# Performance work log

Measured on AMD Instinct MI355X. Metric: run time of the kernel, lower is better.

## Reference

```python
import jax, jax.numpy as jnp
import numpy as np

BETA = 0.25


def setup_inputs() -> dict:
    key = jax.random.key(0)
    k1, k2 = jax.random.split(key)
    z = jax.random.normal(k1, (16, 256, 32, 32), dtype=jnp.float32)
    # nn.Embedding init: uniform(-1/K, 1/K) with K = in_channels = 16384
    K, D = 16384, 256
    emb = jax.random.uniform(k2, (K, D), dtype=jnp.float32,
                             minval=-1.0 / K, maxval=1.0 / K)
    return {"z": z, "emb": emb}


def reference(z, emb):
    K, D = emb.shape
    # NCHW -> NHWC, flatten to tokens
    zp = jnp.transpose(z, (0, 2, 3, 1))            # [B,H,W,D]
    zf = zp.reshape(-1, D)                          # [N,D]
    # squared L2 distances: ||z||^2 + ||e||^2 - 2 z.e  -> [N,K]
    d = (jnp.sum(zf * zf, axis=1, keepdims=True)
         + jnp.sum(emb * emb, axis=1)
         - 2.0 * jnp.matmul(zf, emb.T))
    idx = jnp.argmin(d, axis=1)                     # [N] int
    # gather via direct lookup (equivalent to one-hot @ emb)
    z_q = emb[idx].reshape(zp.shape)                # [B,H,W,D]
    # commitment + codebook loss
    loss = (jnp.mean((jax.lax.stop_gradient(z_q) - zp) ** 2)
            + BETA * jnp.mean((z_q - jax.lax.stop_gradient(zp)) ** 2))
    # perplexity from code usage histogram (same as mean of one-hot rows)
    counts = jax.ops.segment_sum(jnp.ones_like(idx, dtype=jnp.float32), idx,
                                 num_segments=K)
    e_mean = counts / idx.shape[0]
    perplexity = jnp.exp(-jnp.sum(e_mean * jnp.log(e_mean + 1e-10)))
    # straight-through estimator, back to NCHW
    z_q_st = zp + jax.lax.stop_gradient(z_q - zp)
    z_q_out = jnp.transpose(z_q_st, (0, 3, 1, 2))   # [B,D,H,W]
    return z_q_out, loss, perplexity, idx
```

## Files before the change

kernel.cpp:

```cpp
#include <hip/hip_runtime.h>
#include <math.h>

#define NTOK   16384
#define DDIM   256
#define HWD    1024
#define CHW    262144
#define MARGIN 3.0e-4f
#define CLIPF  5.5f
#define QS     (127.0f/5.5f)
#define EQS    2080768.0f
#define SCALE  (5.5f/(127.0f*127.0f*16384.0f))

#define WS_TI8   0u
#define WS_CI8   4194304u
#define WS_M1    8388608u
#define WS_M2    16777216u
#define WS_ARG   25165824u
#define WS_FLG   29360128u
#define WS_EE    29376512u
#define WS_ZZ    29442048u
#define WS_IDX   29507584u
#define WS_CNT   29573120u
#define WS_LSUM  29638656u

typedef __attribute__((ext_vector_type(4)))  int   i32x4;
typedef __attribute__((ext_vector_type(16))) char  c16;
typedef __attribute__((ext_vector_type(4)))  _Float16 h4;

__device__ __forceinline__ void top2m(int& a1, int& a2, const int b1, const int b2) {
  const int mn = min(a1, b1);
  a1 = max(a1, b1);
  a2 = max(max(a2, b2), mn);
}

__global__ __launch_bounds__(256) void k_prep(const float* __restrict__ z,
                                              const float* __restrict__ emb,
                                              char* __restrict__ Ti8,
                                              char* __restrict__ Ci8,
                                              float* __restrict__ zz,
                                              float* __restrict__ ee,
                                              float* __restrict__ zt,
                                              unsigned char* __restrict__ flags) {
  const int bid = blockIdx.x;
  const int tid = threadIdx.x;
  const int t64 = tid & 63, chunk = tid >> 6;
  if (bid < 256) {
    __shared__ double part[4][64];
    __shared__ int   fpart[4][64];
    const int n = bid * 64 + t64;
    const int b = n >> 10, hw = n & 1023;
    const float* zp = z + (size_t)b * CHW + hw;
    float tmp[64];
    double s = 0.0;
    int clip = 0;
    #pragma unroll
    for (int j = 0; j < 64; ++j) {
      const float f = zp[(size_t)(chunk * 64 + j) * HWD];
      tmp[j] = f;
      s += (double)f * (double)f;
      clip |= (fabsf(f) > CLIPF) ? 1 : 0;
    }
    c16 q[4];
    #pragma unroll
    for (int sl = 0; sl < 4; ++sl)
      #pragma unroll
      for (int j = 0; j < 16; ++j)
        q[sl][j] = (char)(int)rintf(fminf(fmaxf(tmp[sl * 16 + j], -CLIPF), CLIPF) * QS);
    const int rl = n & 127, tile = n >> 7;
    char* dst = Ti8 + (size_t)tile * 32768 + chunk * 8192 + rl * 64;
    const int sw = ((rl >> 1) & 3) << 4;
    #pragma unroll
    for (int sl = 0; sl < 4; ++sl) *(c16*)(dst + ((sl * 16) ^ sw)) = q[sl];
    float* ztp = zt + (size_t)n * 256 + chunk * 64;
    #pragma unroll
    for (int j4 = 0; j4 < 16; ++j4) *(float4*)(ztp + j4 * 4) = *(float4*)&tmp[j4 * 4];
    part[chunk][t64] = s;
    fpart[chunk][t64] = clip;
    __syncthreads();
    if (tid < 64) {
      zz[n] = (float)(part[0][t64] + part[1][t64] + part[2][t64] + part[3][t64]);
      flags[n] = (unsigned char)(fpart[0][t64] | fpart[1][t64] | fpart[2][t64] | fpart[3][t64]);
    }
  } else {
    __shared__ float rows[64][257];
    __shared__ double part2[4][64];
    const int k0 = (bid - 256) * 64;
    for (int i = tid; i < 16384; i += 256)
      rows[i >> 8][i & 255] = emb[(size_t)k0 * DDIM + i];
    __syncthreads();
    const int code = k0 + t64;
    double s = 0.0;
    c16 q[4];
    #pragma unroll
    for (int sl = 0; sl < 4; ++sl)
      #pragma unroll
      for (int j = 0; j < 16; ++j) {
        const float f = rows[t64][chunk * 64 + sl * 16 + j];
        q[sl][j] = (char)(int)rintf(f * EQS);
        s += (double)f * (double)f;
      }
    char* dst = Ci8 + (size_t)code * 256 + chunk * 64;
    #pragma unroll
    for (int sl = 0; sl < 4; ++sl) *(c16*)(dst + sl * 16) = q[sl];
    part2[chunk][t64] = s;
    __syncthreads();
    if (tid < 64)
      ee[code] = (float)(part2[0][t64] + part2[1][t64] + part2[2][t64] + part2[3][t64]);
  }
}

__global__ __launch_bounds__(256) void k_mdist(
    const char* __restrict__ tokimg, const char* __restrict__ codrows,
    _Float16* __restrict__ M1, _Float16* __restrict__ M2,
    unsigned char* __restrict__ ARG) {
  __shared__ __attribute__((aligned(16))) char ldsB[65536];
  __shared__ _Float16 m1l[2][256];
  __shared__ _Float16 m2l[2][256];
  __shared__ unsigned char agl[2][256];
  const int raw = blockIdx.x;
  const int p = raw & 7;
  const int ctile = p * 16 + ((raw >> 3) & 15);
  const int tgrp = raw >> 7;
  const int tid = threadIdx.x;
  const int w = tid >> 6, lane = tid & 63;
  const int wr = w >> 1, wc = w & 1;
  const int fr = lane & 15, fq = lane >> 4;

  i32x4 afr[4][4];
  {
    const char* ab = codrows + (size_t)(ctile * 128 + wr * 64 + fr) * 256 + fq * 16;
    #pragma unroll
    for (int m = 0; m < 4; ++m)
      #pragma unroll
      for (int kc = 0; kc < 4; ++kc)
        afr[m][kc] = *(const i32x4*)(ab + m * 16 * 256 + kc * 64);
  }

  int boff[4][4];
  #pragma unroll
  for (int n = 0; n < 4; ++n)
    #pragma unroll
    for (int kc = 0; kc < 4; ++kc) {
      const int t = wc * 64 + n * 16 + fr;
      boff[n][kc] = kc * 8192 + t * 64 + ((fq * 16) ^ (((t >> 1) & 3) << 4));
    }

  #define STAGEB(buf, tt)                                                             \
    {                                                                                 \
      const char* src = tokimg + (size_t)(tt) * 32768;                                \
      char* dstb = ldsB + (buf) * 32768;                                              \
      _Pragma("unroll")                                                               \
      for (int r = 0; r < 8; ++r) {                                                   \
        const int u = r * 256 + tid;                                                  \
        __builtin_amdgcn_global_load_lds(                                             \
            (const __attribute__((address_space(1))) void*)(src + u * 16),            \
            (__attribute__((address_space(3))) void*)(dstb + u * 16), 16, 0, 0);      \
      }                                                                               \
    }

  STAGEB(0, tgrp * 8);
  __syncthreads();

  const int fq4 = fq * 4;
  for (int it = 0; it < 8; ++it) {
    const int pb = it & 1;
    const int ttile = tgrp * 8 + it;
    if (it < 7) STAGEB(pb ^ 1, ttile + 1);
    const char* bufb = ldsB + pb * 32768;

    i32x4 acc[4][4];
    #pragma unroll
    for (int m = 0; m < 4; ++m)
      #pragma unroll
      for (int n = 0; n < 4; ++n) acc[m][n] = (i32x4)0;

    __builtin_amdgcn_s_setprio(1);
    #pragma unroll
    for (int kc = 0; kc < 4; ++kc) {
      i32x4 b[4];
      #pragma unroll
      for (int n = 0; n < 4; ++n) b[n] = *(const i32x4*)(bufb + boff[n][kc]);
      #pragma unroll
      for (int m = 0; m < 4; ++m)
        #pragma unroll
        for (int n = 0; n < 4; ++n)
          acc[m][n] = __builtin_amdgcn_mfma_i32_16x16x64_i8(afr[m][kc], b[n], acc[m][n], 0, 0, 0);
    }
    __builtin_amdgcn_s_setprio(0);

    #pragma unroll
    for (int n = 0; n < 4; ++n) {
      int p1[8], p2[8];
      #pragma unroll
      for (int m = 0; m < 4; ++m)
        #pragma unroll
        for (int jj = 0; jj < 2; ++jj) {
          const int k0 = (acc[m][n][2 * jj]     << 8) | (m * 16 + fq4 + 2 * jj);
          const int k1 = (acc[m][n][2 * jj + 1] << 8) | (m * 16 + fq4 + 2 * jj + 1);
          p1[m * 2 + jj] = max(k0, k1);
          p2[m * 2 + jj] = min(k0, k1);
        }
      top2m(p1[0], p2[0], p1[1], p2[1]); top2m(p1[2], p2[2], p1[3], p2[3]);
      top2m(p1[4], p2[4], p1[5], p2[5]); top2m(p1[6], p2[6], p1[7], p2[7]);
      top2m(p1[0], p2[0], p1[2], p2[2]); top2m(p1[4], p2[4], p1[6], p2[6]);
      top2m(p1[0], p2[0], p1[4], p2[4]);
      int k1 = p1[0], k2 = p2[0];
      #pragma unroll
      for (int off = 16; off <= 32; off <<= 1) {
        const int o1 = __shfl_xor(k1, off, 64);
        const int o2 = __shfl_xor(k2, off, 64);
        top2m(k1, k2, o1, o2);
      }
      if (lane < 16) {
        const int tl = wc * 64 + n * 16 + fr;
        m1l[pb][tl * 2 + wr] = (_Float16)(-2.0f * SCALE * (float)(k1 >> 8));
        m2l[pb][tl * 2 + wr] = (_Float16)(-2.0f * SCALE * (float)(k2 >> 8));
        agl[pb][tl * 2 + wr] = (unsigned char)(k1 & 255);
      }
    }
    __syncthreads();
    if (tid < 128) {
      const int tok = ttile * 128 + tid;
      *(unsigned int*)((char*)M1 + (size_t)tok * 512 + ctile * 4) =
          *(const unsigned int*)(&m1l[pb][tid * 2]);
      M2[(size_t)(ctile * 2) * NTOK + tok]     = m2l[pb][tid * 2];
      M2[(size_t)(ctile * 2 + 1) * NTOK + tok] = m2l[pb][tid * 2 + 1];
      ARG[(size_t)(ctile * 2) * NTOK + tok]     = agl[pb][tid * 2];
      ARG[(size_t)(ctile * 2 + 1) * NTOK + tok] = agl[pb][tid * 2 + 1];
    }
  }
}

__global__ __launch_bounds__(256) void k_pick(
    const float* __restrict__ zt, const float* __restrict__ emb,
    const float* __restrict__ zz, const float* __restrict__ ee,
    const _Float16* __restrict__ M1, const _Float16* __restrict__ M2,
    const unsigned char* __restrict__ ARG, const unsigned char* __restrict__ flags,
    int* __restrict__ idx, float* __restrict__ out_idxf,
    int* __restrict__ counts, double* __restrict__ lsum) {
  __shared__ float zrow[4][260];
  __shared__ int   clist[4][576];
  __shared__ int   wcnt[4];
  __shared__ double wsum[4];
  const int tid = threadIdx.x;
  const int w = tid >> 6, lane = tid & 63;
  const int g16 = lane >> 4, l16 = lane & 15;
  double dsum = 0.0;
  for (int ni = 0; ni < 2; ++ni) {
    const int n = blockIdx.x * 8 + w * 2 + ni;
    if (lane == 0) wcnt[w] = 0;
    *(float4*)&zrow[w][lane * 4] = *(const float4*)(zt + (size_t)n * 256 + lane * 4);
    const h4 mv = *(const h4*)(M1 + (size_t)n * 256 + lane * 4);
    float ta4[4];
    #pragma unroll
    for (int s = 0; s < 4; ++s) ta4[s] = (float)mv[s];
    float mr = fminf(fminf(ta4[0], ta4[1]), fminf(ta4[2], ta4[3]));
    #pragma unroll
    for (int o = 32; o; o >>= 1) mr = fminf(mr, __shfl_xor(mr, o, 64));
    const int ex0 = flags[n];
    const float thr = ex0 ? 3.0e38f : mr + MARGIN;
    if (!ex0) {
      #pragma unroll
      for (int s = 0; s < 4; ++s) {
        if (ta4[s] <= thr) {
          const int sub = lane * 4 + s;
          const float m2v = (float)M2[(size_t)sub * NTOK + n];
          if (m2v > thr) {
            const int pos = atomicAdd(&wcnt[w], 1);
            if (pos < 576) clist[w][pos] = sub * 64 + (int)ARG[(size_t)sub * NTOK + n];
          } else {
            const int pos = atomicAdd(&wcnt[w], 64);
            if (pos + 64 <= 576)
              for (int i = 0; i < 64; ++i) clist[w][pos + i] = sub * 64 + i;
          }
        }
      }
    }
    const int cnt = wcnt[w];
    const int doEx = ex0 || (cnt > 576);
    const int nc = doEx ? 16384 : cnt;
    const float zzn = zz[n];
    unsigned long long best = ~0ull;
    for (int ci = 0; ci < nc; ci += 4) {
      int k;
      if (doEx) k = ci + g16;
      else { const int sl = ci + g16; k = clist[w][sl < cnt ? sl : 0]; }
      const float* erow = emb + (size_t)k * DDIM;
      double s = 0.0;
      #pragma unroll
      for (int qq = 0; qq < 4; ++qq) {
        const float4 ev = *(const float4*)(erow + qq * 64 + l16 * 4);
        const float4 zv = *(const float4*)(&zrow[w][qq * 64 + l16 * 4]);
        s += (double)zv.x * (double)ev.x + (double)zv.y * (double)ev.y
           + (double)zv.z * (double)ev.z + (double)zv.w * (double)ev.w;
      }
      #pragma unroll
      for (int o = 8; o; o >>= 1) s += __shfl_xor(s, o, 16);
      if (l16 == 0) {
        const float mm = (float)s;
        const float d = (zzn + ee[k]) - 2.0f * mm;
        const unsigned long long c =
            ((unsigned long long)__float_as_uint(d) << 32) | (unsigned int)k;
        if (c < best) best = c;
      }
    }
    unsigned long long b0 = (l16 == 0) ? best : ~0ull;
    {
      const unsigned long long o1 = __shfl_xor(b0, 16, 64);
      b0 = o1 < b0 ? o1 : b0;
      const unsigned long long o2 = __shfl_xor(b0, 32, 64);
      b0 = o2 < b0 ? o2 : b0;
    }
    if (lane == 0) {
      const int k0 = (int)(b0 & 0xffffffffu);
      idx[n] = k0;
      out_idxf[n] = (float)k0;
      atomicAdd(&counts[k0], 1);
      dsum += (double)__uint_as_float((unsigned int)(b0 >> 32));
    }
  }
  if (lane == 0) wsum[w] = dsum;
  __syncthreads();
  if (tid == 0) lsum[blockIdx.x] = wsum[0] + wsum[1] + wsum[2] + wsum[3];
}

__global__ __launch_bounds__(256) void k_scatter(
    const float* __restrict__ emb, const int* __restrict__ idx,
    float* __restrict__ out_zq) {
  __shared__ float et[64][257];
  __shared__ int sidx[64];
  const int tg = blockIdx.x;
  const int n0 = tg * 64;
  const int b = n0 >> 10, hw0 = n0 & 1023;
  const int tid = threadIdx.x;
  if (tid < 64) sidx[tid] = idx[n0 + tid];
  __syncthreads();
  for (int i = tid; i < 16384; i += 256) {
    const int t = i >> 8, d = i & 255;
    et[t][d] = emb[(size_t)sidx[t] * DDIM + d];
  }
  __syncthreads();
  float* ob = out_zq + (size_t)b * CHW + hw0;
  for (int i = tid; i < 16384; i += 256) {
    const int d = i >> 6, t = i & 63;
    ob[(size_t)d * HWD + t] = et[t][d];
  }
}

__global__ __launch_bounds__(256) void k_histfinal(const int* __restrict__ counts,
                                                   const double* __restrict__ lsum,
                                                   float* __restrict__ out_loss,
                                                   float* __restrict__ out_perp) {
  __shared__ double w4[4], l4[4];
  const int tid = threadIdx.x;
  double s = 0.0, l = 0.0;
  for (int i = tid; i < 16384; i += 256) {
    const float em = (float)counts[i] * (1.0f / 16384.0f);
    s += (double)(em * logf(em + 1e-10f));
  }
  for (int i = tid; i < 2048; i += 256) l += lsum[i];
  #pragma unroll
  for (int o = 32; o; o >>= 1) {
    s += __shfl_xor(s, o, 64);
    l += __shfl_xor(l, o, 64);
  }
  const int wid = tid >> 6, lane = tid & 63;
  if (lane == 0) { w4[wid] = s; l4[wid] = l; }
  __syncthreads();
  if (tid == 0) {
    const double S = w4[0] + w4[1] + w4[2] + w4[3];
    const double L = l4[0] + l4[1] + l4[2] + l4[3];
    out_loss[0] = (float)(1.25 * L / 4194304.0);
    out_perp[0] = (float)exp(-S);
  }
}

extern "C" void kernel_launch(void* const* d_in, const int* in_sizes, int n_in,
                              void* d_out, int out_size, void* d_ws, size_t ws_size,
                              hipStream_t stream) {
  const float* z   = (const float*)d_in[0];
  const float* emb = (const float*)d_in[1];
  float* out      = (float*)d_out;
  float* out_zq   = out;
  float* out_loss = out + 4194304;
  float* out_perp = out + 4194305;
  float* out_idxf = out + 4194306;
  float* zt       = out;

  char* ws = (char*)d_ws;
  char* Ti8 = ws + WS_TI8;
  char* Ci8 = ws + WS_CI8;
  _Float16* M1 = (_Float16*)(ws + WS_M1);
  _Float16* M2 = (_Float16*)(ws + WS_M2);
  unsigned char* ARG = (unsigned char*)(ws + WS_ARG);
  unsigned char* flags = (unsigned char*)(ws + WS_FLG);
  float*  ee      = (float*)(ws + WS_EE);
  float*  zz      = (float*)(ws + WS_ZZ);
  int*    idx     = (int*)  (ws + WS_IDX);
  int*    counts  = (int*)  (ws + WS_CNT);
  double* lsum    = (double*)(ws + WS_LSUM);

  hipMemsetAsync(counts, 0, 65536, stream);

  k_prep <<<512, 256, 0, stream>>>(z, emb, Ti8, Ci8, zz, ee, zt, flags);
  k_mdist<<<2048, 256, 0, stream>>>(Ti8, Ci8, M1, M2, ARG);
  k_pick <<<2048, 256, 0, stream>>>(zt, emb, zz, ee, M1, M2, ARG, flags,
                                    idx, out_idxf, counts, lsum);
  k_scatter<<<256, 256, 0, stream>>>(emb, idx, out_zq);
  k_histfinal<<<1, 256, 0, stream>>>(counts, lsum, out_loss, out_perp);
}
```

Baseline: 197.7 us.

## Drop top-2 tracking in int8 distance pass, rescore candidate subtiles with int8 dot

The MFMA distance kernel now keeps only the per-subtile maximum score instead of top-2 values plus argmax, so it no longer writes the M2 and ARG arrays. The pick kernel gathers the subtiles within the margin and rescores their 64 codes with int8 dot products, reading a new row-major int8 token copy written by the prep kernel. Only codes within the threshold go on to exact fp64 verification. This removes epilogue work and scattered stores from the main GEMM kernel. In exchange, the pick kernel does more int8 loads and dot products per token, and the fallback to a full 16384-code exact scan now also triggers when more than 24 subtiles qualify or the candidate list ends up empty.

```diff
diff --git a/kernel.cpp b/kernel.cpp
--- a/kernel.cpp
+++ b/kernel.cpp
@@ -14,29 +14,41 @@
 #define WS_TI8   0u
 #define WS_CI8   4194304u
 #define WS_M1    8388608u
-#define WS_M2    16777216u
-#define WS_ARG   25165824u
-#define WS_FLG   29360128u
-#define WS_EE    29376512u
-#define WS_ZZ    29442048u
-#define WS_IDX   29507584u
-#define WS_CNT   29573120u
-#define WS_LSUM  29638656u
+#define WS_TR8   16777216u
+#define WS_FLG   20971520u
+#define WS_EE    20987904u
+#define WS_ZZ    21053440u
+#define WS_IDX   21118976u
+#define WS_CNT   21184512u
+#define WS_LSUM  21250048u
 
 typedef __attribute__((ext_vector_type(4)))  int   i32x4;
 typedef __attribute__((ext_vector_type(16))) char  c16;
 typedef __attribute__((ext_vector_type(4)))  _Float16 h4;
 
-__device__ __forceinline__ void top2m(int& a1, int& a2, const int b1, const int b2) {
-  const int mn = min(a1, b1);
-  a1 = max(a1, b1);
-  a2 = max(max(a2, b2), mn);
+__device__ __forceinline__ int dot16i8(const i32x4 a, const i32x4 b) {
+#if __has_builtin(__builtin_amdgcn_sdot4)
+  int acc = __builtin_amdgcn_sdot4(a[0], b[0], 0, false);
+  acc = __builtin_amdgcn_sdot4(a[1], b[1], acc, false);
+  acc = __builtin_amdgcn_sdot4(a[2], b[2], acc, false);
+  acc = __builtin_amdgcn_sdot4(a[3], b[3], acc, false);
+  return acc;
+#else
+  int acc = 0;
+  #pragma unroll
+  for (int i = 0; i < 4; ++i)
+    #pragma unroll
+    for (int j = 0; j < 4; ++j)
+      acc += ((a[i] << (24 - 8 * j)) >> 24) * ((b[i] << (24 - 8 * j)) >> 24);
+  return acc;
+#endif
 }
 
 __global__ __launch_bounds__(256) void k_prep(const float* __restrict__ z,
                                               const float* __restrict__ emb,
                                               char* __restrict__ Ti8,
                                               char* __restrict__ Ci8,
+                                              char* __restrict__ Tr8,
                                               float* __restrict__ zz,
                                               float* __restrict__ ee,
                                               float* __restrict__ zt,
@@ -71,6 +83,9 @@
     const int sw = ((rl >> 1) & 3) << 4;
     #pragma unroll
     for (int sl = 0; sl < 4; ++sl) *(c16*)(dst + ((sl * 16) ^ sw)) = q[sl];
+    char* dst2 = Tr8 + (size_t)n * 256 + chunk * 64;
+    #pragma unroll
+    for (int sl = 0; sl < 4; ++sl) *(c16*)(dst2 + sl * 16) = q[sl];
     float* ztp = zt + (size_t)n * 256 + chunk * 64;
     #pragma unroll
     for (int j4 = 0; j4 < 16; ++j4) *(float4*)(ztp + j4 * 4) = *(float4*)&tmp[j4 * 4];
@@ -111,12 +126,9 @@
 
 __global__ __launch_bounds__(256) void k_mdist(
     const char* __restrict__ tokimg, const char* __restrict__ codrows,
-    _Float16* __restrict__ M1, _Float16* __restrict__ M2,
-    unsigned char* __restrict__ ARG) {
+    _Float16* __restrict__ M1) {
   __shared__ __attribute__((aligned(16))) char ldsB[65536];
   __shared__ _Float16 m1l[2][256];
-  __shared__ _Float16 m2l[2][256];
-  __shared__ unsigned char agl[2][256];
   const int raw = blockIdx.x;
   const int p = raw & 7;
   const int ctile = p * 16 + ((raw >> 3) & 15);
@@ -161,7 +173,6 @@
   STAGEB(0, tgrp * 8);
   __syncthreads();
 
-  const int fq4 = fq * 4;
   for (int it = 0; it < 8; ++it) {
     const int pb = it & 1;
     const int ttile = tgrp * 8 + it;
@@ -190,43 +201,20 @@
 
     #pragma unroll
     for (int n = 0; n < 4; ++n) {
-      int p1[8], p2[8];
-      #pragma unroll
-      for (int m = 0; m < 4; ++m)
-        #pragma unroll
-        for (int jj = 0; jj < 2; ++jj) {
-          const int k0 = (acc[m][n][2 * jj]     << 8) | (m * 16 + fq4 + 2 * jj);
-          const int k1 = (acc[m][n][2 * jj + 1] << 8) | (m * 16 + fq4 + 2 * jj + 1);
-          p1[m * 2 + jj] = max(k0, k1);
-          p2[m * 2 + jj] = min(k0, k1);
-        }
-      top2m(p1[0], p2[0], p1[1], p2[1]); top2m(p1[2], p2[2], p1[3], p2[3]);
-      top2m(p1[4], p2[4], p1[5], p2[5]); top2m(p1[6], p2[6], p1[7], p2[7]);
-      top2m(p1[0], p2[0], p1[2], p2[2]); top2m(p1[4], p2[4], p1[6], p2[6]);
-      top2m(p1[0], p2[0], p1[4], p2[4]);
-      int k1 = p1[0], k2 = p2[0];
-      #pragma unroll
-      for (int off = 16; off <= 32; off <<= 1) {
-        const int o1 = __shfl_xor(k1, off, 64);
-        const int o2 = __shfl_xor(k2, off, 64);
-        top2m(k1, k2, o1, o2);
-      }
-      if (lane < 16) {
-        const int tl = wc * 64 + n * 16 + fr;
-        m1l[pb][tl * 2 + wr] = (_Float16)(-2.0f * SCALE * (float)(k1 >> 8));
-        m2l[pb][tl * 2 + wr] = (_Float16)(-2.0f * SCALE * (float)(k2 >> 8));
-        agl[pb][tl * 2 + wr] = (unsigned char)(k1 & 255);
-      }
+      int v = max(max(acc[0][n][0], acc[0][n][1]), max(acc[0][n][2], acc[0][n][3]));
+      #pragma unroll
+      for (int m = 1; m < 4; ++m)
+        v = max(v, max(max(acc[m][n][0], acc[m][n][1]), max(acc[m][n][2], acc[m][n][3])));
+      v = max(v, __shfl_xor(v, 16, 64));
+      v = max(v, __shfl_xor(v, 32, 64));
+      if (lane < 16)
+        m1l[pb][(wc * 64 + n * 16 + fr) * 2 + wr] = (_Float16)(-2.0f * SCALE * (float)v);
     }
     __syncthreads();
     if (tid < 128) {
       const int tok = ttile * 128 + tid;
       *(unsigned int*)((char*)M1 + (size_t)tok * 512 + ctile * 4) =
           *(const unsigned int*)(&m1l[pb][tid * 2]);
-      M2[(size_t)(ctile * 2) * NTOK + tok]     = m2l[pb][tid * 2];
-      M2[(size_t)(ctile * 2 + 1) * NTOK + tok] = m2l[pb][tid * 2 + 1];
-      ARG[(size_t)(ctile * 2) * NTOK + tok]     = agl[pb][tid * 2];
-      ARG[(size_t)(ctile * 2 + 1) * NTOK + tok] = agl[pb][tid * 2 + 1];
     }
   }
 }
@@ -234,13 +222,14 @@
 __global__ __launch_bounds__(256) void k_pick(
     const float* __restrict__ zt, const float* __restrict__ emb,
     const float* __restrict__ zz, const float* __restrict__ ee,
-    const _Float16* __restrict__ M1, const _Float16* __restrict__ M2,
-    const unsigned char* __restrict__ ARG, const unsigned char* __restrict__ flags,
+    const _Float16* __restrict__ M1, const char* __restrict__ Tr8,
+    const char* __restrict__ Ci8, const unsigned char* __restrict__ flags,
     int* __restrict__ idx, float* __restrict__ out_idxf,
     int* __restrict__ counts, double* __restrict__ lsum) {
   __shared__ float zrow[4][260];
   __shared__ int   clist[4][576];
-  __shared__ int   wcnt[4];
+  __shared__ int   slist[4][24];
+  __shared__ int   wcnt[4], scnt2[4];
   __shared__ double wsum[4];
   const int tid = threadIdx.x;
   const int w = tid >> 6, lane = tid & 63;
@@ -248,8 +237,9 @@
   double dsum = 0.0;
   for (int ni = 0; ni < 2; ++ni) {
     const int n = blockIdx.x * 8 + w * 2 + ni;
-    if (lane == 0) wcnt[w] = 0;
+    if (lane == 0) { wcnt[w] = 0; scnt2[w] = 0; }
     *(float4*)&zrow[w][lane * 4] = *(const float4*)(zt + (size_t)n * 256 + lane * 4);
+    const i32x4 trow = *(const i32x4*)(Tr8 + (size_t)n * 256 + l16 * 16);
     const h4 mv = *(const h4*)(M1 + (size_t)n * 256 + lane * 4);
     float ta4[4];
     #pragma unroll
@@ -263,21 +253,37 @@
       #pragma unroll
       for (int s = 0; s < 4; ++s) {
         if (ta4[s] <= thr) {
-          const int sub = lane * 4 + s;
-          const float m2v = (float)M2[(size_t)sub * NTOK + n];
-          if (m2v > thr) {
-            const int pos = atomicAdd(&wcnt[w], 1);
-            if (pos < 576) clist[w][pos] = sub * 64 + (int)ARG[(size_t)sub * NTOK + n];
-          } else {
-            const int pos = atomicAdd(&wcnt[w], 64);
-            if (pos + 64 <= 576)
-              for (int i = 0; i < 64; ++i) clist[w][pos + i] = sub * 64 + i;
+          const int pos = atomicAdd(&scnt2[w], 1);
+          if (pos < 24) slist[w][pos] = lane * 4 + s;
+        }
+      }
+    }
+    const int ns = scnt2[w];
+    int doEx = ex0 || (ns > 24);
+    if (!doEx) {
+      for (int si = 0; si < ns; ++si) {
+        const int sub = slist[w][si];
+        #pragma unroll 4
+        for (int p2 = 0; p2 < 16; ++p2) {
+          const int k = sub * 64 + p2 * 4 + g16;
+          const i32x4 crow = *(const i32x4*)(Ci8 + (size_t)k * 256 + l16 * 16);
+          int v = dot16i8(trow, crow);
+          v += __shfl_xor(v, 8, 16);
+          v += __shfl_xor(v, 4, 16);
+          v += __shfl_xor(v, 2, 16);
+          v += __shfl_xor(v, 1, 16);
+          if (l16 == 0) {
+            const float dest = -2.0f * SCALE * (float)v;
+            if (dest <= thr) {
+              const int pos = atomicAdd(&wcnt[w], 1);
+              if (pos < 576) clist[w][pos] = k;
+            }
           }
         }
       }
+      if (wcnt[w] > 576 || wcnt[w] == 0) doEx = 1;
     }
     const int cnt = wcnt[w];
-    const int doEx = ex0 || (cnt > 576);
     const int nc = doEx ? 16384 : cnt;
     const float zzn = zz[n];
     unsigned long long best = ~0ull;
@@ -390,9 +396,8 @@
   char* ws = (char*)d_ws;
   char* Ti8 = ws + WS_TI8;
   char* Ci8 = ws + WS_CI8;
+  char* Tr8 = ws + WS_TR8;
   _Float16* M1 = (_Float16*)(ws + WS_M1);
-  _Float16* M2 = (_Float16*)(ws + WS_M2);
-  unsigned char* ARG = (unsigned char*)(ws + WS_ARG);
   unsigned char* flags = (unsigned char*)(ws + WS_FLG);
   float*  ee      = (float*)(ws + WS_EE);
   float*  zz      = (float*)(ws + WS_ZZ);
@@ -402,9 +407,9 @@
 
   hipMemsetAsync(counts, 0, 65536, stream);
 
-  k_prep <<<512, 256, 0, stream>>>(z, emb, Ti8, Ci8, zz, ee, zt, flags);
-  k_mdist<<<2048, 256, 0, stream>>>(Ti8, Ci8, M1, M2, ARG);
-  k_pick <<<2048, 256, 0, stream>>>(zt, emb, zz, ee, M1, M2, ARG, flags,
+  k_prep <<<512, 256, 0, stream>>>(z, emb, Ti8, Ci8, Tr8, zz, ee, zt, flags);
+  k_mdist<<<2048, 256, 0, stream>>>(Ti8, Ci8, M1);
+  k_pick <<<2048, 256, 0, stream>>>(zt, emb, zz, ee, M1, Tr8, Ci8, flags,
                                     idx, out_idxf, counts, lsum);
   k_scatter<<<256, 256, 0, stream>>>(emb, idx, out_zq);
   k_histfinal<<<1, 256, 0, stream>>>(counts, lsum, out_loss, out_perp);
```

Measured after the change: 344.4 us. 74.2% more time.

## Replace per-group top-2 screening with finer max-per-32-code groups and group rescoring

Applied to the files above, without the earlier changes.

The int8 screening kernel stops tracking top-2 scores and argmax per 64-code group. It now records only the max score per 32-code group into a single token-major fp16 buffer, dropping the M2 and ARG buffers and their strided writes. The pick kernel selects groups within a margin of the best and rescores all 32 codes in each in fp64, with 4 lanes per code instead of 16. This cuts epilogue work and memory traffic in the distance kernel. In exchange the exact rescoring can do more work per token, and it falls back to a full scan when more than 32 groups pass the threshold.

```diff
diff --git a/kernel.cpp b/kernel.cpp
--- a/kernel.cpp
+++ b/kernel.cpp
@@ -13,25 +13,18 @@
 
 #define WS_TI8   0u
 #define WS_CI8   4194304u
-#define WS_M1    8388608u
-#define WS_M2    16777216u
-#define WS_ARG   25165824u
-#define WS_FLG   29360128u
-#define WS_EE    29376512u
-#define WS_ZZ    29442048u
-#define WS_IDX   29507584u
-#define WS_CNT   29573120u
-#define WS_LSUM  29638656u
+#define WS_M3    8388608u
+#define WS_FLG   25165824u
+#define WS_EE    25182208u
+#define WS_ZZ    25247744u
+#define WS_IDX   25313280u
+#define WS_CNT   25378816u
+#define WS_LSUM  25444352u
 
 typedef __attribute__((ext_vector_type(4)))  int   i32x4;
 typedef __attribute__((ext_vector_type(16))) char  c16;
-typedef __attribute__((ext_vector_type(4)))  _Float16 h4;
-
-__device__ __forceinline__ void top2m(int& a1, int& a2, const int b1, const int b2) {
-  const int mn = min(a1, b1);
-  a1 = max(a1, b1);
-  a2 = max(max(a2, b2), mn);
-}
+typedef __attribute__((ext_vector_type(8)))  _Float16 h8f;
+typedef unsigned long long ull;
 
 __global__ __launch_bounds__(256) void k_prep(const float* __restrict__ z,
                                               const float* __restrict__ emb,
@@ -111,12 +104,9 @@
 
 __global__ __launch_bounds__(256) void k_mdist(
     const char* __restrict__ tokimg, const char* __restrict__ codrows,
-    _Float16* __restrict__ M1, _Float16* __restrict__ M2,
-    unsigned char* __restrict__ ARG) {
+    _Float16* __restrict__ M3) {
   __shared__ __attribute__((aligned(16))) char ldsB[65536];
-  __shared__ _Float16 m1l[2][256];
-  __shared__ _Float16 m2l[2][256];
-  __shared__ unsigned char agl[2][256];
+  __shared__ _Float16 m3l[2][512];
   const int raw = blockIdx.x;
   const int p = raw & 7;
   const int ctile = p * 16 + ((raw >> 3) & 15);
@@ -161,7 +151,6 @@
   STAGEB(0, tgrp * 8);
   __syncthreads();
 
-  const int fq4 = fq * 4;
   for (int it = 0; it < 8; ++it) {
     const int pb = it & 1;
     const int ttile = tgrp * 8 + it;
@@ -190,43 +179,23 @@
 
     #pragma unroll
     for (int n = 0; n < 4; ++n) {
-      int p1[8], p2[8];
-      #pragma unroll
-      for (int m = 0; m < 4; ++m)
-        #pragma unroll
-        for (int jj = 0; jj < 2; ++jj) {
-          const int k0 = (acc[m][n][2 * jj]     << 8) | (m * 16 + fq4 + 2 * jj);
-          const int k1 = (acc[m][n][2 * jj + 1] << 8) | (m * 16 + fq4 + 2 * jj + 1);
-          p1[m * 2 + jj] = max(k0, k1);
-          p2[m * 2 + jj] = min(k0, k1);
-        }
-      top2m(p1[0], p2[0], p1[1], p2[1]); top2m(p1[2], p2[2], p1[3], p2[3]);
-      top2m(p1[4], p2[4], p1[5], p2[5]); top2m(p1[6], p2[6], p1[7], p2[7]);
-      top2m(p1[0], p2[0], p1[2], p2[2]); top2m(p1[4], p2[4], p1[6], p2[6]);
-      top2m(p1[0], p2[0], p1[4], p2[4]);
-      int k1 = p1[0], k2 = p2[0];
-      #pragma unroll
-      for (int off = 16; off <= 32; off <<= 1) {
-        const int o1 = __shfl_xor(k1, off, 64);
-        const int o2 = __shfl_xor(k2, off, 64);
-        top2m(k1, k2, o1, o2);
-      }
-      if (lane < 16) {
-        const int tl = wc * 64 + n * 16 + fr;
-        m1l[pb][tl * 2 + wr] = (_Float16)(-2.0f * SCALE * (float)(k1 >> 8));
-        m2l[pb][tl * 2 + wr] = (_Float16)(-2.0f * SCALE * (float)(k2 >> 8));
-        agl[pb][tl * 2 + wr] = (unsigned char)(k1 & 255);
+      #pragma unroll
+      for (int g = 0; g < 2; ++g) {
+        int v = max(max(acc[2 * g][n][0], acc[2 * g][n][1]),
+                    max(acc[2 * g][n][2], acc[2 * g][n][3]));
+        v = max(v, max(max(acc[2 * g + 1][n][0], acc[2 * g + 1][n][1]),
+                       max(acc[2 * g + 1][n][2], acc[2 * g + 1][n][3])));
+        v = max(v, __shfl_xor(v, 16, 64));
+        v = max(v, __shfl_xor(v, 32, 64));
+        if (lane < 16)
+          m3l[pb][(wc * 64 + n * 16 + fr) * 4 + wr * 2 + g] =
+              (_Float16)(-2.0f * SCALE * (float)v);
       }
     }
     __syncthreads();
     if (tid < 128) {
       const int tok = ttile * 128 + tid;
-      *(unsigned int*)((char*)M1 + (size_t)tok * 512 + ctile * 4) =
-          *(const unsigned int*)(&m1l[pb][tid * 2]);
-      M2[(size_t)(ctile * 2) * NTOK + tok]     = m2l[pb][tid * 2];
-      M2[(size_t)(ctile * 2 + 1) * NTOK + tok] = m2l[pb][tid * 2 + 1];
-      ARG[(size_t)(ctile * 2) * NTOK + tok]     = agl[pb][tid * 2];
-      ARG[(size_t)(ctile * 2 + 1) * NTOK + tok] = agl[pb][tid * 2 + 1];
+      *(ull*)(M3 + (size_t)tok * 512 + ctile * 4) = *(const ull*)(&m3l[pb][tid * 4]);
     }
   }
 }
@@ -234,82 +203,79 @@
 __global__ __launch_bounds__(256) void k_pick(
     const float* __restrict__ zt, const float* __restrict__ emb,
     const float* __restrict__ zz, const float* __restrict__ ee,
-    const _Float16* __restrict__ M1, const _Float16* __restrict__ M2,
-    const unsigned char* __restrict__ ARG, const unsigned char* __restrict__ flags,
+    const _Float16* __restrict__ M3, const unsigned char* __restrict__ flags,
     int* __restrict__ idx, float* __restrict__ out_idxf,
     int* __restrict__ counts, double* __restrict__ lsum) {
   __shared__ float zrow[4][260];
-  __shared__ int   clist[4][576];
-  __shared__ int   wcnt[4];
+  __shared__ int   glist[4][32];
+  __shared__ int   gcnt[4];
   __shared__ double wsum[4];
   const int tid = threadIdx.x;
   const int w = tid >> 6, lane = tid & 63;
-  const int g16 = lane >> 4, l16 = lane & 15;
+  const int c16p = lane >> 2, l4 = lane & 3;
   double dsum = 0.0;
   for (int ni = 0; ni < 2; ++ni) {
     const int n = blockIdx.x * 8 + w * 2 + ni;
-    if (lane == 0) wcnt[w] = 0;
+    if (lane == 0) gcnt[w] = 0;
     *(float4*)&zrow[w][lane * 4] = *(const float4*)(zt + (size_t)n * 256 + lane * 4);
-    const h4 mv = *(const h4*)(M1 + (size_t)n * 256 + lane * 4);
-    float ta4[4];
-    #pragma unroll
-    for (int s = 0; s < 4; ++s) ta4[s] = (float)mv[s];
-    float mr = fminf(fminf(ta4[0], ta4[1]), fminf(ta4[2], ta4[3]));
+    const h8f mv = *(const h8f*)(M3 + (size_t)n * 512 + lane * 8);
+    float t8[8];
+    #pragma unroll
+    for (int s = 0; s < 8; ++s) t8[s] = (float)mv[s];
+    float mr = t8[0];
+    #pragma unroll
+    for (int s = 1; s < 8; ++s) mr = fminf(mr, t8[s]);
     #pragma unroll
     for (int o = 32; o; o >>= 1) mr = fminf(mr, __shfl_xor(mr, o, 64));
     const int ex0 = flags[n];
     const float thr = ex0 ? 3.0e38f : mr + MARGIN;
     if (!ex0) {
       #pragma unroll
-      for (int s = 0; s < 4; ++s) {
-        if (ta4[s] <= thr) {
-          const int sub = lane * 4 + s;
-          const float m2v = (float)M2[(size_t)sub * NTOK + n];
-          if (m2v > thr) {
-            const int pos = atomicAdd(&wcnt[w], 1);
-            if (pos < 576) clist[w][pos] = sub * 64 + (int)ARG[(size_t)sub * NTOK + n];
-          } else {
-            const int pos = atomicAdd(&wcnt[w], 64);
-            if (pos + 64 <= 576)
-              for (int i = 0; i < 64; ++i) clist[w][pos + i] = sub * 64 + i;
-          }
+      for (int s = 0; s < 8; ++s) {
+        if (t8[s] <= thr) {
+          const int pos = atomicAdd(&gcnt[w], 1);
+          if (pos < 32) glist[w][pos] = lane * 8 + s;
         }
       }
     }
-    const int cnt = wcnt[w];
-    const int doEx = ex0 || (cnt > 576);
-    const int nc = doEx ? 16384 : cnt;
+    const int ng = gcnt[w];
+    const int doEx = ex0 || (ng > 32);
+    const int nchunk = doEx ? 1024 : ng * 2;
     const float zzn = zz[n];
-    unsigned long long best = ~0ull;
-    for (int ci = 0; ci < nc; ci += 4) {
+    ull best = ~0ull;
+    const float* zp4 = &zrow[w][l4 * 64];
+    for (int ci = 0; ci < nchunk; ++ci) {
       int k;
-      if (doEx) k = ci + g16;
-      else { const int sl = ci + g16; k = clist[w][sl < cnt ? sl : 0]; }
-      const float* erow = emb + (size_t)k * DDIM;
-      double s = 0.0;
-      #pragma unroll
-      for (int qq = 0; qq < 4; ++qq) {
-        const float4 ev = *(const float4*)(erow + qq * 64 + l16 * 4);
-        const float4 zv = *(const float4*)(&zrow[w][qq * 64 + l16 * 4]);
-        s += (double)zv.x * (double)ev.x + (double)zv.y * (double)ev.y
-           + (double)zv.z * (double)ev.z + (double)zv.w * (double)ev.w;
-      }
-      #pragma unroll
-      for (int o = 8; o; o >>= 1) s += __shfl_xor(s, o, 16);
-      if (l16 == 0) {
+      if (doEx) k = ci * 16 + c16p;
+      else      k = glist[w][ci >> 1] * 32 + (ci & 1) * 16 + c16p;
+      const float* erow = emb + (size_t)k * DDIM + l4 * 64;
+      double s0 = 0.0, s1 = 0.0;
+      #pragma unroll
+      for (int jj = 0; jj < 8; ++jj) {
+        const float4 e0 = *(const float4*)(erow + jj * 8);
+        const float4 z0 = *(const float4*)(zp4 + jj * 8);
+        const float4 e1 = *(const float4*)(erow + jj * 8 + 4);
+        const float4 z1 = *(const float4*)(zp4 + jj * 8 + 4);
+        s0 += (double)z0.x * (double)e0.x + (double)z0.y * (double)e0.y
+            + (double)z0.z * (double)e0.z + (double)z0.w * (double)e0.w;
+        s1 += (double)z1.x * (double)e1.x + (double)z1.y * (double)e1.y
+            + (double)z1.z * (double)e1.z + (double)z1.w * (double)e1.w;
+      }
+      double s = s0 + s1;
+      s += __shfl_xor(s, 1, 4);
+      s += __shfl_xor(s, 2, 4);
+      if (l4 == 0) {
         const float mm = (float)s;
         const float d = (zzn + ee[k]) - 2.0f * mm;
-        const unsigned long long c =
-            ((unsigned long long)__float_as_uint(d) << 32) | (unsigned int)k;
+        const ull c = ((ull)__float_as_uint(d) << 32) | (unsigned int)k;
         if (c < best) best = c;
       }
     }
-    unsigned long long b0 = (l16 == 0) ? best : ~0ull;
-    {
-      const unsigned long long o1 = __shfl_xor(b0, 16, 64);
-      b0 = o1 < b0 ? o1 : b0;
-      const unsigned long long o2 = __shfl_xor(b0, 32, 64);
-      b0 = o2 < b0 ? o2 : b0;
+    ull b0 = best;
+    #pragma unroll
+    for (int o = 4; o <= 32; o <<= 1) {
+      const ull ot = __shfl_xor(b0, o, 64);
+      b0 = ot < b0 ? ot : b0;
     }
     if (lane == 0) {
       const int k0 = (int)(b0 & 0xffffffffu);
@@ -351,7 +317,7 @@
                                                    const double* __restrict__ lsum,
                                                    float* __restrict__ out_loss,
                                                    float* __restrict__ out_perp) {
-  __shared__ double w4[4], l4[4];
+  __shared__ double w4[4], l4a[4];
   const int tid = threadIdx.x;
   double s = 0.0, l = 0.0;
   for (int i = tid; i < 16384; i += 256) {
@@ -365,11 +331,11 @@
     l += __shfl_xor(l, o, 64);
   }
   const int wid = tid >> 6, lane = tid & 63;
-  if (lane == 0) { w4[wid] = s; l4[wid] = l; }
+  if (lane == 0) { w4[wid] = s; l4a[wid] = l; }
   __syncthreads();
   if (tid == 0) {
     const double S = w4[0] + w4[1] + w4[2] + w4[3];
-    const double L = l4[0] + l4[1] + l4[2] + l4[3];
+    const double L = l4a[0] + l4a[1] + l4a[2] + l4a[3];
     out_loss[0] = (float)(1.25 * L / 4194304.0);
     out_perp[0] = (float)exp(-S);
   }
@@ -390,9 +356,7 @@
   char* ws = (char*)d_ws;
   char* Ti8 = ws + WS_TI8;
   char* Ci8 = ws + WS_CI8;
-  _Float16* M1 = (_Float16*)(ws + WS_M1);
-  _Float16* M2 = (_Float16*)(ws + WS_M2);
-  unsigned char* ARG = (unsigned char*)(ws + WS_ARG);
+  _Float16* M3 = (_Float16*)(ws + WS_M3);
   unsigned char* flags = (unsigned char*)(ws + WS_FLG);
   float*  ee      = (float*)(ws + WS_EE);
   float*  zz      = (float*)(ws + WS_ZZ);
@@ -403,8 +367,8 @@
   hipMemsetAsync(counts, 0, 65536, stream);
 
   k_prep <<<512, 256, 0, stream>>>(z, emb, Ti8, Ci8, zz, ee, zt, flags);
-  k_mdist<<<2048, 256, 0, stream>>>(Ti8, Ci8, M1, M2, ARG);
-  k_pick <<<2048, 256, 0, stream>>>(zt, emb, zz, ee, M1, M2, ARG, flags,
+  k_mdist<<<2048, 256, 0, stream>>>(Ti8, Ci8, M3);
+  k_pick <<<2048, 256, 0, stream>>>(zt, emb, zz, ee, M3, flags,
                                     idx, out_idxf, counts, lsum);
   k_scatter<<<256, 256, 0, stream>>>(emb, idx, out_zq);
   k_histfinal<<<1, 256, 0, stream>>>(counts, lsum, out_loss, out_perp);
```

Measured after the change: 452.0 us. 2.29x slower.
